# Optimization experiments

Hardware: AMD Instinct MI355X
Metric: run time of the kernel (lower is better)

The kernel has to match this reference:

```python
import jax, jax.numpy as jnp
import numpy as np

IOU_THRESH = 0.6
IMG_SIZE = 2048.0


def _iou_matrix(boxes):
    # boxes: [N, 4] as (x1, y1, x2, y2)
    x1, y1, x2, y2 = boxes[:, 0], boxes[:, 1], boxes[:, 2], boxes[:, 3]
    area = jnp.maximum(x2 - x1, 0.0) * jnp.maximum(y2 - y1, 0.0)  # [N]
    ix1 = jnp.maximum(x1[:, None], x1[None, :])
    iy1 = jnp.maximum(y1[:, None], y1[None, :])
    ix2 = jnp.minimum(x2[:, None], x2[None, :])
    iy2 = jnp.minimum(y2[:, None], y2[None, :])
    inter = jnp.maximum(ix2 - ix1, 0.0) * jnp.maximum(iy2 - iy1, 0.0)  # [N, N]
    union = area[:, None] + area[None, :] - inter
    return inter / jnp.maximum(union, 1e-9)


def _nms_keep(boxes, thresh):
    # Greedy NMS in the given (score-sorted) order; returns a [N] bool keep mask.
    n = boxes.shape[0]
    iou = _iou_matrix(boxes)  # [N, N] -- dominant memory traffic
    idx = jnp.arange(n)

    def step(suppressed, i):
        keep_i = jnp.logical_not(suppressed[i])
        # a kept box suppresses all LATER boxes with IoU > thresh
        suppressed = suppressed | (keep_i & (idx > i) & (iou[i] > thresh))
        return suppressed, keep_i

    _, keep = jax.lax.scan(step, jnp.zeros((n,), dtype=bool), idx)
    return keep


def _make_boxes(kc, ks, n):
    c = jax.random.uniform(kc, (n, 2), minval=0.0, maxval=IMG_SIZE)
    s = jax.random.uniform(ks, (n, 2), minval=10.0, maxval=120.0)
    return jnp.concatenate([c - s / 2, c + s / 2], axis=1)  # [n, 4]


def setup_inputs() -> dict:
    key = jax.random.key(0)
    k1, k2, k3, k4, k5, k6 = jax.random.split(key, 6)
    N = 8192  # vstacked detections across projections
    M = 8192  # vstacked RPN rois across projections
    det_boxes = _make_boxes(k1, k2, N)
    cls_scores = jax.random.normal(k3, (N, 4), dtype=jnp.float32)  # 4 TL classes, class 0 = invalid
    proj_id = jnp.zeros((N, 1), dtype=jnp.float32)
    detections = jnp.concatenate([proj_id, det_boxes, cls_scores], axis=1)  # [N, 9]
    rpn_boxes = _make_boxes(k4, k5, M)
    objness = jax.random.uniform(k6, (M, 1), dtype=jnp.float32)
    rpn_data = jnp.concatenate([jnp.zeros((M, 1), dtype=jnp.float32), rpn_boxes, objness], axis=1)  # [M, 6]
    return {"detections": detections, "rpn_data": rpn_data}


def reference(detections, rpn_data):
    # detect(): NMS(0.6) on detections[:, 1:5] and on rpn_data[:, 1:5]
    keep_det = _nms_keep(detections[:, 1:5], IOU_THRESH)  # [N] bool
    keep_rpn = _nms_keep(rpn_data[:, 1:5], IOU_THRESH)    # [M] bool
    # forward(): split surviving detections into valid (tl_type != 0) / invalid
    tl_types = jnp.argmax(detections[:, 5:], axis=1)
    valid_mask = keep_det & (tl_types != 0)
    invalid_mask = keep_det & (tl_types == 0)
    # fixed-shape (jit-friendly) masked outputs instead of data-dependent gather
    valid_detections = detections * valid_mask[:, None].astype(detections.dtype)
    invalid_detections = detections * invalid_mask[:, None].astype(detections.dtype)
    rpn_attack_data = rpn_data * keep_rpn[:, None].astype(rpn_data.dtype)
    return valid_detections, invalid_detections, rpn_attack_data
```

## Files before the change

### kernel.cpp

```cpp
#include <hip/hip_runtime.h>


constexpr int NROWS = 8192;
constexpr int NKW   = 256;
constexpr unsigned BCAP = 1536;
constexpr unsigned ACAP = 512;
constexpr unsigned RCAP = 2048;
constexpr unsigned ELDS = 16384;
#define IOU_T 0.6f

constexpr size_t OFF_EDGES = 4096;

__global__ __launch_bounds__(256) void scanpair_kernel(
    const float* __restrict__ det, const float* __restrict__ rpn,
    unsigned* __restrict__ cnts, unsigned* __restrict__ edges)
{
  const int cellid = blockIdx.x, set = blockIdx.y;
  const float* src  = (set == 0) ? det : rpn;
  const int    strd = (set == 0) ? 9 : 6;
  unsigned* myedges = edges + ((size_t)(set * 256 + cellid)) * RCAP;
  const int cx = cellid & 15, cy = cellid >> 4;

  __shared__ float Bx1[BCAP], By1[BCAP], Bx2[BCAP], By2[BCAP], Bar[BCAP];
  __shared__ unsigned Bid[BCAP];
  __shared__ unsigned aList[ACAP];
  __shared__ unsigned bCnt, aCnt, eCnt, ovf;

  const int t = threadIdx.x;
  if (t == 0) { bCnt = 0u; aCnt = 0u; eCnt = 0u; ovf = 0u; }
  __syncthreads();

  for (int r = t; r < NROWS; r += 256) {
    const float* p = src + (size_t)r * strd + 1;
    const float x1 = p[0], y1 = p[1], x2 = p[2], y2 = p[3];
    const float cxe = 0.5f * (x1 + x2), cye = 0.5f * (y1 + y2);
    const int ccx = min(15, max(0, (int)(cxe * (1.0f / 128.0f))));
    const int ccy = min(15, max(0, (int)(cye * (1.0f / 128.0f))));
    const int dx = ccx - cx, dy = ccy - cy;
    if (dx >= -1 && dx <= 1 && dy >= -1 && dy <= 1) {
      const unsigned s = atomicAdd(&bCnt, 1u);
      if (s < BCAP) {
        Bx1[s] = x1; By1[s] = y1; Bx2[s] = x2; By2[s] = y2;
        Bar[s] = fmaxf(x2 - x1, 0.0f) * fmaxf(y2 - y1, 0.0f);
        Bid[s] = (unsigned)r;
        if (dx == 0 && dy == 0) {
          const unsigned as = atomicAdd(&aCnt, 1u);
          if (as < ACAP) aList[as] = s; else atomicOr(&ovf, 1u);
        }
      } else atomicOr(&ovf, 1u);
    }
  }
  __syncthreads();

  const unsigned nb = min(bCnt, BCAP);
  const unsigned na = min(aCnt, ACAP);

  if (!ovf) {
    const unsigned tot = na * nb;
    for (unsigned p = t; p < tot; p += 256) {
      const unsigned ai = p / nb, x = p - ai * nb;
      const unsigned s = aList[ai];
      const unsigned ia = Bid[s], ib = Bid[x];
      if (ia < ib) {
        const float ix1 = fmaxf(Bx1[s], Bx1[x]), iy1 = fmaxf(By1[s], By1[x]);
        const float ix2 = fminf(Bx2[s], Bx2[x]), iy2 = fminf(By2[s], By2[x]);
        const float inter = fmaxf(ix2 - ix1, 0.0f) * fmaxf(iy2 - iy1, 0.0f);
        if (inter > 0.0f) {
          const float uni = Bar[s] + Bar[x] - inter;
          const float iou = inter / fmaxf(uni, 1e-9f);
          if (iou > IOU_T) {
            const unsigned slot = atomicAdd(&eCnt, 1u);
            if (slot < RCAP) myedges[slot] = (ia << 13) | ib;
          }
        }
      }
    }
  } else {
    for (int ra = 0; ra < NROWS; ++ra) {
      const float* pa = src + (size_t)ra * strd + 1;
      const float ax1 = pa[0], ay1 = pa[1], ax2 = pa[2], ay2 = pa[3];
      const float cxe = 0.5f * (ax1 + ax2), cye = 0.5f * (ay1 + ay2);
      const int ccx = min(15, max(0, (int)(cxe * (1.0f / 128.0f))));
      const int ccy = min(15, max(0, (int)(cye * (1.0f / 128.0f))));
      if (ccx != cx || ccy != cy) continue;
      const float aar = fmaxf(ax2 - ax1, 0.0f) * fmaxf(ay2 - ay1, 0.0f);
      for (int rb = t; rb < NROWS; rb += 256) {
        if ((unsigned)ra >= (unsigned)rb) continue;
        const float* pb = src + (size_t)rb * strd + 1;
        const float bx1 = pb[0], by1 = pb[1], bx2 = pb[2], by2 = pb[3];
        const float ix1 = fmaxf(ax1, bx1), iy1 = fmaxf(ay1, by1);
        const float ix2 = fminf(ax2, bx2), iy2 = fminf(ay2, by2);
        const float inter = fmaxf(ix2 - ix1, 0.0f) * fmaxf(iy2 - iy1, 0.0f);
        if (inter > 0.0f) {
          const float bar = fmaxf(bx2 - bx1, 0.0f) * fmaxf(by2 - by1, 0.0f);
          const float uni = aar + bar - inter;
          const float iou = inter / fmaxf(uni, 1e-9f);
          if (iou > IOU_T) {
            const unsigned slot = atomicAdd(&eCnt, 1u);
            if (slot < RCAP) myedges[slot] = ((unsigned)ra << 13) | (unsigned)rb;
          }
        }
      }
    }
  }
  __syncthreads();
  if (t == 0) cnts[set * 256 + cellid] = min(eCnt, RCAP);
}

__global__ __launch_bounds__(1024) void solve_epi_kernel(
    const float* __restrict__ det, const float* __restrict__ rpn,
    const unsigned* __restrict__ cnts, const unsigned* __restrict__ edges,
    float* __restrict__ out)
{
  const int blk = blockIdx.x;
  const int set = blk >> 4;
  const int slice = blk & 15;
  const unsigned* gedges = edges + (size_t)set * 256 * RCAP;

  __shared__ unsigned eL[ELDS];
  __shared__ unsigned rcnt[256], roff[256];
  __shared__ unsigned kbuf[2][NKW];
  __shared__ int changed[2];
  __shared__ unsigned Etot_sh;

  const int t = threadIdx.x;
  if (t < 256) rcnt[t] = min(cnts[set * 256 + t], RCAP);
  __syncthreads();

  if (t < 64) {
    const unsigned h0 = rcnt[4 * t], h1 = rcnt[4 * t + 1];
    const unsigned h2 = rcnt[4 * t + 2], h3 = rcnt[4 * t + 3];
    const unsigned lsum = h0 + h1 + h2 + h3;
    unsigned incl = lsum;
    #pragma unroll
    for (int d = 1; d < 64; d <<= 1) {
      const unsigned v = __shfl_up(incl, d);
      if (t >= d) incl += v;
    }
    const unsigned base = incl - lsum;
    roff[4 * t] = base;           roff[4 * t + 1] = base + h0;
    roff[4 * t + 2] = base + h0 + h1; roff[4 * t + 3] = base + h0 + h1 + h2;
    if (t == 63) Etot_sh = incl;
  }
  if (t < NKW) kbuf[0][t] = 0xFFFFFFFFu;
  __syncthreads();

  const unsigned Etot = Etot_sh;
  const bool cached = (Etot <= ELDS);
  if (cached && t < 256) {
    const unsigned c = rcnt[t], o = roff[t];
    for (unsigned k = 0; k < c; ++k) eL[o + k] = gedges[(size_t)t * RCAP + k];
  }
  __syncthreads();

  int cur = 0;
  for (int round = 0; round < NROWS + 8; ++round) {
    const int nxt = cur ^ 1;
    if (t == 0) changed[round & 1] = 0;
    if (t < NKW) kbuf[nxt][t] = 0xFFFFFFFFu;
    __syncthreads();

    if (cached) {
      for (unsigned e = t; e < Etot; e += 1024) {
        const unsigned pk = eL[e];
        const unsigned i = pk >> 13, j = pk & 8191u;
        if ((kbuf[cur][i >> 5] >> (i & 31)) & 1u)
          atomicAnd(&kbuf[nxt][j >> 5], ~(1u << (j & 31)));
      }
    } else {
      for (unsigned r = (unsigned)t >> 2; r < 256u; r += 256u) {
        const unsigned c = rcnt[r];
        for (unsigned k = (unsigned)t & 3u; k < c; k += 4u) {
          const unsigned pk = gedges[(size_t)r * RCAP + k];
          const unsigned i = pk >> 13, j = pk & 8191u;
          if ((kbuf[cur][i >> 5] >> (i & 31)) & 1u)
            atomicAnd(&kbuf[nxt][j >> 5], ~(1u << (j & 31)));
        }
      }
    }
    __syncthreads();

    if (t < NKW && kbuf[nxt][t] != kbuf[cur][t]) changed[round & 1] = 1;
    __syncthreads();

    cur = nxt;
    if (!changed[round & 1]) break;
  }

  const int r0 = slice * 512;
  if (set == 0) {
    for (int i = r0 + t; i < r0 + 512; i += 1024) {
      const bool kd = (kbuf[cur][i >> 5] >> (i & 31)) & 1u;
      const float* p = det + (size_t)i * 9;
      const float sc0 = p[5], sc1 = p[6], sc2 = p[7], sc3 = p[8];
      int am = 0; float best = sc0;
      if (sc1 > best) { best = sc1; am = 1; }
      if (sc2 > best) { best = sc2; am = 2; }
      if (sc3 > best) { best = sc3; am = 3; }
      const float vm = (kd && am != 0) ? 1.0f : 0.0f;
      const float im = (kd && am == 0) ? 1.0f : 0.0f;
      float* o0 = out + (size_t)i * 9;
      float* o1 = out + (size_t)NROWS * 9 + (size_t)i * 9;
      #pragma unroll
      for (int c = 0; c < 9; ++c) { const float v = p[c]; o0[c] = v * vm; o1[c] = v * im; }
    }
  } else {
    for (int i = r0 + t; i < r0 + 512; i += 1024) {
      const bool kr = (kbuf[cur][i >> 5] >> (i & 31)) & 1u;
      const float rm = kr ? 1.0f : 0.0f;
      const float* q = rpn + (size_t)i * 6;
      float* o2 = out + (size_t)NROWS * 18 + (size_t)i * 6;
      #pragma unroll
      for (int c = 0; c < 6; ++c) o2[c] = q[c] * rm;
    }
  }
}

extern "C" void kernel_launch(void* const* d_in, const int* in_sizes, int n_in,
                              void* d_out, int out_size, void* d_ws, size_t ws_size,
                              hipStream_t stream)
{
  const float* det = (const float*)d_in[0];
  const float* rpn = (const float*)d_in[1];
  float* out = (float*)d_out;

  char* ws = (char*)d_ws;
  unsigned* cnts  = (unsigned*)ws;
  unsigned* edges = (unsigned*)(ws + OFF_EDGES);

  dim3 g1(256, 2);
  scanpair_kernel<<<g1, 256, 0, stream>>>(det, rpn, cnts, edges);
  solve_epi_kernel<<<32, 1024, 0, stream>>>(det, rpn, cnts, edges, out);
}
```

Before: 88.67 us.

## Fuse edge-building and NMS solve into one cooperative kernel with grid sync

Merges the spatial-cell IoU edge kernel and the iterative keep-mask solver into one cooperative launch of 512 blocks of 256 threads, separated by a grid-wide sync. Each block then redundantly runs the fixed-point solve for its set and writes only its 32-row slice of the output, which spreads the epilogue over more blocks. This removes the second launch and the gap between kernels, at the cost of running the serial solve with 256 threads instead of 1024 and a smaller shared edge cache (8192 edges), so the slower global-memory path is taken more often. The two-kernel path is kept as a fallback if the cooperative launch fails.

Measured after the change: 160.2 us. +80.6%, slower.

```diff
diff --git a/kernel.cpp b/kernel.cpp
--- a/kernel.cpp
+++ b/kernel.cpp
@@ -1,4 +1,7 @@
 #include <hip/hip_runtime.h>
+#include <hip/hip_cooperative_groups.h>
+
+namespace cg = cooperative_groups;
 
 
 constexpr int NROWS = 8192;
@@ -6,10 +9,239 @@
 constexpr unsigned BCAP = 1536;
 constexpr unsigned ACAP = 512;
 constexpr unsigned RCAP = 2048;
-constexpr unsigned ELDS = 16384;
+constexpr unsigned ELDS = 8192;
 #define IOU_T 0.6f
 
 constexpr size_t OFF_EDGES = 4096;
+
+constexpr int SMW = 9732;
+
+__global__ __launch_bounds__(256) void fused_kernel(
+    const float* __restrict__ det, const float* __restrict__ rpn,
+    unsigned* __restrict__ cnts, unsigned* __restrict__ edges,
+    float* __restrict__ out)
+{
+  __shared__ unsigned sm[SMW];
+
+  const int blk = blockIdx.x;
+  const int cellid = blk & 255;
+  const int set    = blk >> 8;
+  const int t = threadIdx.x;
+
+  {
+    float*    Bx1 = (float*)&sm[0];
+    float*    By1 = (float*)&sm[1536];
+    float*    Bx2 = (float*)&sm[3072];
+    float*    By2 = (float*)&sm[4608];
+    float*    Bar = (float*)&sm[6144];
+    unsigned* Bid = &sm[7680];
+    unsigned* aList = &sm[9216];
+    unsigned* cw = &sm[9728];
+
+    const float* src  = (set == 0) ? det : rpn;
+    const int    strd = (set == 0) ? 9 : 6;
+    unsigned* myedges = edges + ((size_t)(set * 256 + cellid)) * RCAP;
+    const int cx = cellid & 15, cy = cellid >> 4;
+
+    if (t < 4) cw[t] = 0u;
+    __syncthreads();
+
+    for (int r = t; r < NROWS; r += 256) {
+      const float* p = src + (size_t)r * strd + 1;
+      const float x1 = p[0], y1 = p[1], x2 = p[2], y2 = p[3];
+      const float cxe = 0.5f * (x1 + x2), cye = 0.5f * (y1 + y2);
+      const int ccx = min(15, max(0, (int)(cxe * (1.0f / 128.0f))));
+      const int ccy = min(15, max(0, (int)(cye * (1.0f / 128.0f))));
+      const int dx = ccx - cx, dy = ccy - cy;
+      if (dx >= -1 && dx <= 1 && dy >= -1 && dy <= 1) {
+        const unsigned s = atomicAdd(&cw[0], 1u);
+        if (s < BCAP) {
+          Bx1[s] = x1; By1[s] = y1; Bx2[s] = x2; By2[s] = y2;
+          Bar[s] = fmaxf(x2 - x1, 0.0f) * fmaxf(y2 - y1, 0.0f);
+          Bid[s] = (unsigned)r;
+          if (dx == 0 && dy == 0) {
+            const unsigned as = atomicAdd(&cw[1], 1u);
+            if (as < ACAP) aList[as] = s; else atomicOr(&cw[3], 1u);
+          }
+        } else atomicOr(&cw[3], 1u);
+      }
+    }
+    __syncthreads();
+
+    const unsigned nb = min(cw[0], BCAP);
+    const unsigned na = min(cw[1], ACAP);
+
+    if (!cw[3]) {
+      const unsigned tot = na * nb;
+      for (unsigned p = t; p < tot; p += 256) {
+        const unsigned ai = p / nb, x = p - ai * nb;
+        const unsigned s = aList[ai];
+        const unsigned ia = Bid[s], ib = Bid[x];
+        if (ia < ib) {
+          const float ix1 = fmaxf(Bx1[s], Bx1[x]), iy1 = fmaxf(By1[s], By1[x]);
+          const float ix2 = fminf(Bx2[s], Bx2[x]), iy2 = fminf(By2[s], By2[x]);
+          const float inter = fmaxf(ix2 - ix1, 0.0f) * fmaxf(iy2 - iy1, 0.0f);
+          if (inter > 0.0f) {
+            const float uni = Bar[s] + Bar[x] - inter;
+            const float iou = inter / fmaxf(uni, 1e-9f);
+            if (iou > IOU_T) {
+              const unsigned slot = atomicAdd(&cw[2], 1u);
+              if (slot < RCAP) myedges[slot] = (ia << 13) | ib;
+            }
+          }
+        }
+      }
+    } else {
+      for (int ra = 0; ra < NROWS; ++ra) {
+        const float* pa = src + (size_t)ra * strd + 1;
+        const float ax1 = pa[0], ay1 = pa[1], ax2 = pa[2], ay2 = pa[3];
+        const float cxe = 0.5f * (ax1 + ax2), cye = 0.5f * (ay1 + ay2);
+        const int ccx = min(15, max(0, (int)(cxe * (1.0f / 128.0f))));
+        const int ccy = min(15, max(0, (int)(cye * (1.0f / 128.0f))));
+        if (ccx != cx || ccy != cy) continue;
+        const float aar = fmaxf(ax2 - ax1, 0.0f) * fmaxf(ay2 - ay1, 0.0f);
+        for (int rb = t; rb < NROWS; rb += 256) {
+          if ((unsigned)ra >= (unsigned)rb) continue;
+          const float* pb = src + (size_t)rb * strd + 1;
+          const float bx1 = pb[0], by1 = pb[1], bx2 = pb[2], by2 = pb[3];
+          const float ix1 = fmaxf(ax1, bx1), iy1 = fmaxf(ay1, by1);
+          const float ix2 = fminf(ax2, bx2), iy2 = fminf(ay2, by2);
+          const float inter = fmaxf(ix2 - ix1, 0.0f) * fmaxf(iy2 - iy1, 0.0f);
+          if (inter > 0.0f) {
+            const float bar = fmaxf(bx2 - bx1, 0.0f) * fmaxf(by2 - by1, 0.0f);
+            const float uni = aar + bar - inter;
+            const float iou = inter / fmaxf(uni, 1e-9f);
+            if (iou > IOU_T) {
+              const unsigned slot = atomicAdd(&cw[2], 1u);
+              if (slot < RCAP)
+                myedges[slot] = ((unsigned)ra << 13) | (unsigned)rb;
+            }
+          }
+        }
+      }
+    }
+    __syncthreads();
+    if (t == 0) cnts[set * 256 + cellid] = min(cw[2], RCAP);
+  }
+
+  __threadfence();
+  cg::this_grid().sync();
+
+  {
+    unsigned* eL    = &sm[0];
+    unsigned* rcnt  = &sm[8192];
+    unsigned* roff  = &sm[8448];
+    unsigned* kb0   = &sm[8704];
+    unsigned* kb1   = &sm[8960];
+    unsigned* chg   = &sm[9216];
+    unsigned* etot  = &sm[9218];
+    float*    vmsk  = (float*)&sm[9220];
+    float*    imsk  = (float*)&sm[9252];
+
+    const unsigned* gedges = edges + (size_t)set * 256 * RCAP;
+
+    if (t < 256) rcnt[t] = min(cnts[set * 256 + t], RCAP);
+    __syncthreads();
+
+    if (t < 64) {
+      const unsigned h0 = rcnt[4 * t], h1 = rcnt[4 * t + 1];
+      const unsigned h2 = rcnt[4 * t + 2], h3 = rcnt[4 * t + 3];
+      const unsigned lsum = h0 + h1 + h2 + h3;
+      unsigned incl = lsum;
+      #pragma unroll
+      for (int d = 1; d < 64; d <<= 1) {
+        const unsigned v = __shfl_up(incl, d);
+        if (t >= d) incl += v;
+      }
+      const unsigned base = incl - lsum;
+      roff[4 * t] = base;               roff[4 * t + 1] = base + h0;
+      roff[4 * t + 2] = base + h0 + h1; roff[4 * t + 3] = base + h0 + h1 + h2;
+      if (t == 63) *etot = incl;
+    }
+    if (t < NKW) kb0[t] = 0xFFFFFFFFu;
+    __syncthreads();
+
+    const unsigned Etot = *etot;
+    const bool cached = (Etot <= ELDS);
+    if (cached && t < 256) {
+      const unsigned c = rcnt[t], o = roff[t];
+      for (unsigned k = 0; k < c; ++k) eL[o + k] = gedges[(size_t)t * RCAP + k];
+    }
+    __syncthreads();
+
+    unsigned* kcur = kb0;
+    unsigned* knxt = kb1;
+    for (int round = 0; round < NROWS + 8; ++round) {
+      if (t == 0) chg[round & 1] = 0u;
+      if (t < NKW) knxt[t] = 0xFFFFFFFFu;
+      __syncthreads();
+
+      if (cached) {
+        for (unsigned e = t; e < Etot; e += 256) {
+          const unsigned pk = eL[e];
+          const unsigned i = pk >> 13, j = pk & 8191u;
+          if ((kcur[i >> 5] >> (i & 31)) & 1u)
+            atomicAnd(&knxt[j >> 5], ~(1u << (j & 31)));
+        }
+      } else {
+        for (unsigned r = (unsigned)t >> 2; r < 256u; r += 64u) {
+          const unsigned c = rcnt[r];
+          for (unsigned k = (unsigned)t & 3u; k < c; k += 4u) {
+            const unsigned pk = gedges[(size_t)r * RCAP + k];
+            const unsigned i = pk >> 13, j = pk & 8191u;
+            if ((kcur[i >> 5] >> (i & 31)) & 1u)
+              atomicAnd(&knxt[j >> 5], ~(1u << (j & 31)));
+          }
+        }
+      }
+      __syncthreads();
+
+      if (t < NKW && knxt[t] != kcur[t]) chg[round & 1] = 1u;
+      __syncthreads();
+
+      unsigned* tmp = kcur; kcur = knxt; knxt = tmp;
+      if (!chg[round & 1]) break;
+    }
+
+    const int r0 = cellid * 32;
+    if (set == 0) {
+      if (t < 32) {
+        const int row = r0 + t;
+        const bool kd = (kcur[row >> 5] >> (row & 31)) & 1u;
+        const float* p = det + (size_t)row * 9;
+        const float sc0 = p[5], sc1 = p[6], sc2 = p[7], sc3 = p[8];
+        int am = 0; float best = sc0;
+        if (sc1 > best) { best = sc1; am = 1; }
+        if (sc2 > best) { best = sc2; am = 2; }
+        if (sc3 > best) { best = sc3; am = 3; }
+        vmsk[t] = (kd && am != 0) ? 1.0f : 0.0f;
+        imsk[t] = (kd && am == 0) ? 1.0f : 0.0f;
+      }
+      __syncthreads();
+      const size_t f0 = (size_t)r0 * 9;
+      float* o0 = out + f0;
+      float* o1 = out + (size_t)NROWS * 9 + f0;
+      for (int k = t; k < 32 * 9; k += 256) {
+        const int lr = k / 9;
+        const float v = det[f0 + k];
+        o0[k] = v * vmsk[lr];
+        o1[k] = v * imsk[lr];
+      }
+    } else {
+      if (t < 32) {
+        const int row = r0 + t;
+        const bool kr = (kcur[row >> 5] >> (row & 31)) & 1u;
+        vmsk[t] = kr ? 1.0f : 0.0f;
+      }
+      __syncthreads();
+      const size_t g0 = (size_t)r0 * 6;
+      float* o2 = out + (size_t)NROWS * 18 + g0;
+      for (int k = t; k < 32 * 6; k += 256) {
+        o2[k] = rpn[g0 + k] * vmsk[k / 6];
+      }
+    }
+  }
+}
 
 __global__ __launch_bounds__(256) void scanpair_kernel(
     const float* __restrict__ det, const float* __restrict__ rpn,
@@ -117,7 +349,7 @@
   const int slice = blk & 15;
   const unsigned* gedges = edges + (size_t)set * 256 * RCAP;
 
-  __shared__ unsigned eL[ELDS];
+  __shared__ unsigned eL[16384];
   __shared__ unsigned rcnt[256], roff[256];
   __shared__ unsigned kbuf[2][NKW];
   __shared__ int changed[2];
@@ -138,7 +370,7 @@
       if (t >= d) incl += v;
     }
     const unsigned base = incl - lsum;
-    roff[4 * t] = base;           roff[4 * t + 1] = base + h0;
+    roff[4 * t] = base;               roff[4 * t + 1] = base + h0;
     roff[4 * t + 2] = base + h0 + h1; roff[4 * t + 3] = base + h0 + h1 + h2;
     if (t == 63) Etot_sh = incl;
   }
@@ -146,7 +378,7 @@
   __syncthreads();
 
   const unsigned Etot = Etot_sh;
-  const bool cached = (Etot <= ELDS);
+  const bool cached = (Etot <= 16384u);
   if (cached && t < 256) {
     const unsigned c = rcnt[t], o = roff[t];
     for (unsigned k = 0; k < c; ++k) eL[o + k] = gedges[(size_t)t * RCAP + k];
@@ -228,7 +460,13 @@
   unsigned* cnts  = (unsigned*)ws;
   unsigned* edges = (unsigned*)(ws + OFF_EDGES);
 
-  dim3 g1(256, 2);
-  scanpair_kernel<<<g1, 256, 0, stream>>>(det, rpn, cnts, edges);
-  solve_epi_kernel<<<32, 1024, 0, stream>>>(det, rpn, cnts, edges, out);
+  void* args[] = { (void*)&det, (void*)&rpn, (void*)&cnts, (void*)&edges,
+                   (void*)&out };
+  const hipError_t err = hipLaunchCooperativeKernel(
+      (const void*)fused_kernel, dim3(512), dim3(256), args, 0, stream);
+  if (err != hipSuccess) {
+    dim3 g1(256, 2);
+    scanpair_kernel<<<g1, 256, 0, stream>>>(det, rpn, cnts, edges);
+    solve_epi_kernel<<<32, 1024, 0, stream>>>(det, rpn, cnts, edges, out);
+  }
 }
```
